# Kernel optimization log

Measured on AMD Instinct MI355X. Metric: run time of the kernel, lower is better.

The kernel has to match this reference:

```python
import jax, jax.numpy as jnp
import numpy as np

P = 16  # patch size

def _conv1x1(w, b, h):
    # w: [O, C], h: [B, C, H, W]
    return jnp.einsum('oc,bcij->boij', w, h) + b[None, :, None, None]

def _forward(x, pe_w, pe_b, mix1_w, mix1_b, mix2_w, mix2_b, qc_w, qc_b,
             codebook, dpre1_w, dpre1_b, dpre2_w, dpre2_b, up_w, up_b):
    B, Cin, H, W = x.shape
    Hp, Wp = H // P, W // P
    # --- encoder: non-overlapping patchify conv (kernel=stride=P) ---
    xp = x.reshape(B, Cin, Hp, P, Wp, P)
    h = jnp.einsum('bcipjq,ocpq->boij', xp, pe_w) + pe_b[None, :, None, None]
    h = jax.nn.relu(h)
    h = jax.nn.relu(_conv1x1(mix1_w, mix1_b, h))
    h = _conv1x1(mix2_w, mix2_b, h)
    # quantize_conv_b
    e = _conv1x1(qc_w, qc_b, h)                      # [B, D, Hp, Wp]
    D = e.shape[1]
    z = e.transpose(0, 2, 3, 1).reshape(B, Hp * Wp, D)   # [B, N, D]
    # --- vector quantization: euclidean argmin over codebook ---
    # dist[b,n,k] = |z|^2 - 2 z.c_k + |c_k|^2
    dist = ((z * z).sum(-1, keepdims=True)
            - 2.0 * jnp.einsum('bnd,kd->bnk', z, codebook)
            + (codebook * codebook).sum(-1))
    idx = jnp.argmin(dist, axis=-1)                  # [B, N] int
    q = codebook[idx]                                # [B, N, D]
    # commitment loss (quantize detached, as in VectorQuantize)
    diff = jnp.mean(jnp.square(jax.lax.stop_gradient(q) - z))
    # straight-through estimator
    q = z + jax.lax.stop_gradient(q - z)
    quant = q.reshape(B, Hp, Wp, D).transpose(0, 3, 1, 2)  # [B, D, Hp, Wp]
    # --- decoder ---
    h = jax.nn.relu(_conv1x1(dpre1_w, dpre1_b, quant))
    h = jax.nn.relu(_conv1x1(dpre2_w, dpre2_b, h))
    # unpatchify: ConvTranspose2d kernel=stride=P, torch weight [C, out, P, P]
    Cout = up_w.shape[1]
    dec = jnp.einsum('bcij,copq->boipjq', h, up_w).reshape(B, Cout, Hp * P, Wp * P)
    dec = dec + up_b[None, :, None, None]
    return dec, diff[None], idx

def setup_inputs() -> dict:
    key = jax.random.key(0)
    ks = jax.random.split(key, 16)
    B, Cin, H, W = 32, 3, 256, 256
    C, D, K = 256, 512, 8192
    s = 0.02
    f32 = jnp.float32
    return {
        'x':       jax.random.normal(ks[0], (B, Cin, H, W), f32),
        'pe_w':    jax.random.normal(ks[1], (C, Cin, P, P), f32) * s,
        'pe_b':    jnp.zeros((C,), f32),
        'mix1_w':  jax.random.normal(ks[2], (C, C), f32) * s,
        'mix1_b':  jnp.zeros((C,), f32),
        'mix2_w':  jax.random.normal(ks[3], (C, C), f32) * s,
        'mix2_b':  jnp.zeros((C,), f32),
        'qc_w':    jax.random.normal(ks[4], (D, C), f32) * s,
        'qc_b':    jnp.zeros((D,), f32),
        'codebook': jax.random.normal(ks[5], (K, D), f32),
        'dpre1_w': jax.random.normal(ks[6], (C, D), f32) * s,
        'dpre1_b': jnp.zeros((C,), f32),
        'dpre2_w': jax.random.normal(ks[7], (C, C), f32) * s,
        'dpre2_b': jnp.zeros((C,), f32),
        'up_w':    jax.random.normal(ks[8], (C, Cin, P, P), f32) * s,
        'up_b':    jnp.zeros((Cin,), f32),
    }

def reference(x, pe_w, pe_b, mix1_w, mix1_b, mix2_w, mix2_b, qc_w, qc_b,
              codebook, dpre1_w, dpre1_b, dpre2_w, dpre2_b, up_w, up_b):
    return _forward(x, pe_w, pe_b, mix1_w, mix1_b, mix2_w, mix2_b, qc_w, qc_b,
                    codebook, dpre1_w, dpre1_b, dpre2_w, dpre2_b, up_w, up_b)
```

## Files before the change

kernel.cpp:

```cpp
#include <hip/hip_runtime.h>
#include <hip/hip_bf16.h>
#include <float.h>


#define TOK   8192
#define CBK   8192
#define CBD   512

typedef short  short8v __attribute__((ext_vector_type(8)));
typedef float  f32x4   __attribute__((ext_vector_type(4)));
typedef unsigned short ush;

__device__ __forceinline__ unsigned short f2bf(float x) {
    union { __hip_bfloat16 b; unsigned short u; } c;
    c.b = __float2bfloat16(x);
    return c.u;
}
__device__ __forceinline__ float bf2f(unsigned short h) {
    return __uint_as_float((unsigned)h << 16);
}

__device__ __forceinline__ void gload16(const void* g, void* l) {
    __builtin_amdgcn_global_load_lds(
        (const __attribute__((address_space(1))) unsigned int*)g,
        (__attribute__((address_space(3))) unsigned int*)l, 16, 0, 0);
}

template<int NPASS, int AMODE, int STMODE, bool RELU>
__global__ __launch_bounds__(256)
void gemm_bf2(const ush* __restrict__ Ah, const ush* __restrict__ Al,
              const ush* __restrict__ Bh, const ush* __restrict__ Bl,
              const float* __restrict__ bias,
              float* __restrict__ Cf, ush* __restrict__ Ch, ush* __restrict__ Cl,
              const float* __restrict__ rowidx, int N, int K, int NT)
{
    __shared__ __align__(16) ush AzH[2][128 * 64];
    __shared__ __align__(16) ush AzL[2][128 * 64];
    __shared__ __align__(16) ush BcH[2][64 * 64];
    __shared__ __align__(16) ush BcL[2][64 * 64];

    const int tid = threadIdx.x, lane = tid & 63, wid = tid >> 6;
    const int wr = wid >> 1, wc = wid & 1;
    const int m0 = blockIdx.x * 128, n0 = blockIdx.y * 64;
    const int l15 = lane & 15, l4 = lane >> 4;

    size_t aoff[4];
    int    aldst[4];
    #pragma unroll
    for (int i = 0; i < 4; ++i) {
        const int ci = (wid * 4 + i) * 64 + lane;
        const int r = ci >> 3, p = ci & 7;
        size_t rowbase;
        if constexpr (AMODE == 2) rowbase = (size_t)((int)rowidx[m0 + r]) * K;
        else                      rowbase = (size_t)(m0 + r) * K;
        aoff[i]  = rowbase + ((p ^ (r & 7)) << 3);
        aldst[i] = (wid * 4 + i) * 512;
    }
    size_t boff[2];
    int    bldst[2];
    #pragma unroll
    for (int i = 0; i < 2; ++i) {
        const int ci = (wid * 2 + i) * 64 + lane;
        const int r = ci >> 3, p = ci & 7;
        boff[i]  = (size_t)(n0 + r) * K + ((p ^ (r & 7)) << 3);
        bldst[i] = (wid * 2 + i) * 512;
    }

    auto STAGE = [&](int t, int b) {
        const int k0 = t << 6;
        #pragma unroll
        for (int i = 0; i < 4; ++i) {
            gload16(Ah + aoff[i] + k0, &AzH[b][aldst[i]]);
            gload16(Al + aoff[i] + k0, &AzL[b][aldst[i]]);
        }
        #pragma unroll
        for (int i = 0; i < 2; ++i) {
            gload16(Bh + boff[i] + k0, &BcH[b][bldst[i]]);
            gload16(Bl + boff[i] + k0, &BcL[b][bldst[i]]);
        }
    };

    f32x4 acc[4][2];
    #pragma unroll
    for (int mi = 0; mi < 4; ++mi)
        #pragma unroll
        for (int nj = 0; nj < 2; ++nj)
            acc[mi][nj] = (f32x4){0.f, 0.f, 0.f, 0.f};

    STAGE(0, 0);
    __syncthreads();
    for (int t = 0; t < NT; ++t) {
        const int b = t & 1;
        if (t + 1 < NT) STAGE(t + 1, b ^ 1);
        #pragma unroll
        for (int ks = 0; ks < 2; ++ks) {
            short8v aFh[4], aFl[4];
            #pragma unroll
            for (int mi = 0; mi < 4; ++mi) {
                const int r = wr * 64 + mi * 16 + l15;
                const int off = r * 64 + (((ks * 4 + l4) ^ (r & 7)) << 3);
                aFh[mi] = *(const short8v*)(&AzH[b][off]);
                aFl[mi] = *(const short8v*)(&AzL[b][off]);
            }
            #pragma unroll
            for (int nj = 0; nj < 2; ++nj) {
                const int rn = wc * 32 + nj * 16 + l15;
                const int off = rn * 64 + (((ks * 4 + l4) ^ (rn & 7)) << 3);
                const short8v bh = *(const short8v*)(&BcH[b][off]);
                const short8v bl = *(const short8v*)(&BcL[b][off]);
                #pragma unroll
                for (int mi = 0; mi < 4; ++mi) {
                    acc[mi][nj] = __builtin_amdgcn_mfma_f32_16x16x32_bf16(aFh[mi], bh, acc[mi][nj], 0, 0, 0);
                    acc[mi][nj] = __builtin_amdgcn_mfma_f32_16x16x32_bf16(aFh[mi], bl, acc[mi][nj], 0, 0, 0);
                    acc[mi][nj] = __builtin_amdgcn_mfma_f32_16x16x32_bf16(aFl[mi], bh, acc[mi][nj], 0, 0, 0);
                    if constexpr (NPASS == 4)
                        acc[mi][nj] = __builtin_amdgcn_mfma_f32_16x16x32_bf16(aFl[mi], bl, acc[mi][nj], 0, 0, 0);
                }
            }
        }
        __syncthreads();
    }

    #pragma unroll
    for (int nj = 0; nj < 2; ++nj) {
        const int n = n0 + wc * 32 + nj * 16 + l15;
        const float bv = (STMODE == 2) ? bias[n >> 8] : bias[n];
        #pragma unroll
        for (int mi = 0; mi < 4; ++mi) {
            #pragma unroll
            for (int i = 0; i < 4; ++i) {
                const int m = m0 + wr * 64 + mi * 16 + l4 * 4 + i;
                float v = acc[mi][nj][i] + bv;
                if constexpr (RELU) v = fmaxf(v, 0.f);
                if constexpr (STMODE == 0) {
                    const unsigned short h = f2bf(v);
                    Ch[(size_t)m * N + n] = h;
                    Cl[(size_t)m * N + n] = f2bf(v - bf2f(h));
                } else if constexpr (STMODE == 1) {
                    Cf[(size_t)m * N + n] = v;
                    Ch[(size_t)m * N + n] = f2bf(v);
                } else {
                    const int o = n >> 8, p = (n >> 4) & 15, q = n & 15;
                    const int b2 = m >> 8, ii = (m >> 4) & 15, jj = m & 15;
                    Cf[((size_t)(b2 * 3 + o) * 256 + ii * 16 + p) * 256 + jj * 16 + q] = v;
                }
            }
        }
    }
}

__global__ __launch_bounds__(256)
void vq_scan(const ush* __restrict__ zh, const ush* __restrict__ cbh,
             const float* __restrict__ cnorm, int* __restrict__ cand)
{
    __shared__ __align__(16) ush Az[2][128 * 64];
    __shared__ __align__(16) ush Bc[2][128 * 64];

    const int tid = threadIdx.x, lane = tid & 63, wid = tid >> 6;
    const int wr = wid >> 1, wc = wid & 1;
    const int m0 = blockIdx.x * 128;
    const int cy = blockIdx.y;
    const int l15 = lane & 15, l4 = lane >> 4;

    size_t soff[4];
    int    ldst[4];
    #pragma unroll
    for (int i = 0; i < 4; ++i) {
        const int ci = (wid * 4 + i) * 64 + lane;
        const int r = ci >> 3, p = ci & 7;
        soff[i] = (size_t)r * CBD + ((p ^ (r & 7)) << 3);
        ldst[i] = (wid * 4 + i) * 512;
    }

    auto STAGE = [&](int t, int b) {
        const int chk = t >> 3, k0 = (t & 7) << 6;
        const size_t ab = (size_t)m0 * CBD + k0;
        const size_t bb = (size_t)(cy * 1024 + chk * 128) * CBD + k0;
        #pragma unroll
        for (int i = 0; i < 4; ++i) {
            gload16(zh  + ab + soff[i], &Az[b][ldst[i]]);
            gload16(cbh + bb + soff[i], &Bc[b][ldst[i]]);
        }
    };

    float r1[16], r2[16];
    int   i1[16], i2[16];
    #pragma unroll
    for (int r = 0; r < 16; ++r) { r1[r] = FLT_MAX; r2[r] = FLT_MAX; i1[r] = 0; i2[r] = 0; }

    f32x4 acc[4][4];
    STAGE(0, 0);
    __syncthreads();
    for (int t = 0; t < 64; ++t) {
        const int b = t & 1;
        if (t < 63) STAGE(t + 1, b ^ 1);
        if ((t & 7) == 0) {
            #pragma unroll
            for (int mi = 0; mi < 4; ++mi)
                #pragma unroll
                for (int nj = 0; nj < 4; ++nj)
                    acc[mi][nj] = (f32x4){0.f, 0.f, 0.f, 0.f};
        }
        #pragma unroll
        for (int ks = 0; ks < 2; ++ks) {
            short8v aF[4];
            #pragma unroll
            for (int mi = 0; mi < 4; ++mi) {
                const int r = wr * 64 + mi * 16 + l15;
                aF[mi] = *(const short8v*)(&Az[b][r * 64 + (((ks * 4 + l4) ^ (r & 7)) << 3)]);
            }
            #pragma unroll
            for (int nj = 0; nj < 4; ++nj) {
                const int rn = wc * 64 + nj * 16 + l15;
                const short8v bF = *(const short8v*)(&Bc[b][rn * 64 + (((ks * 4 + l4) ^ (rn & 7)) << 3)]);
                #pragma unroll
                for (int mi = 0; mi < 4; ++mi)
                    acc[mi][nj] = __builtin_amdgcn_mfma_f32_16x16x32_bf16(aF[mi], bF, acc[mi][nj], 0, 0, 0);
            }
        }
        if ((t & 7) == 7) {
            const int c0 = cy * 1024 + (t >> 3) * 128;
            #pragma unroll
            for (int nj = 0; nj < 4; ++nj) {
                const int code = c0 + wc * 64 + nj * 16 + l15;
                const float cn = cnorm[code];
                #pragma unroll
                for (int mi = 0; mi < 4; ++mi) {
                    #pragma unroll
                    for (int i = 0; i < 4; ++i) {
                        const float d = cn - 2.0f * acc[mi][nj][i];
                        const int rr = mi * 4 + i;
                        if (d < r1[rr]) { r2[rr] = r1[rr]; i2[rr] = i1[rr]; r1[rr] = d; i1[rr] = code; }
                        else if (d < r2[rr]) { r2[rr] = d; i2[rr] = code; }
                    }
                }
            }
        }
        __syncthreads();
    }

    #pragma unroll
    for (int r = 0; r < 16; ++r) {
        float a1 = r1[r], a2 = r2[r];
        int   x1 = i1[r], x2 = i2[r];
        #pragma unroll
        for (int off = 1; off < 16; off <<= 1) {
            const float b1 = __shfl_xor(a1, off), b2 = __shfl_xor(a2, off);
            const int   y1 = __shfl_xor(x1, off), y2 = __shfl_xor(x2, off);
            if (b1 < a1) {
                const float n2 = (a1 < b2) ? a1 : b2;
                const int   m2 = (a1 < b2) ? x1 : y2;
                a2 = n2; x2 = m2; a1 = b1; x1 = y1;
            } else {
                if (b1 < a2) { a2 = b1; x2 = y1; }
            }
        }
        r1[r] = a1; i1[r] = x1; r2[r] = a2; i2[r] = x2;
    }
    if (l15 == 0) {
        const int slot = cy * 2 + wc;
        #pragma unroll
        for (int mi = 0; mi < 4; ++mi)
            #pragma unroll
            for (int i = 0; i < 4; ++i) {
                const int tok = m0 + wr * 64 + mi * 16 + l4 * 4 + i;
                cand[(slot * 2 + 0) * TOK + tok] = i1[mi * 4 + i];
                cand[(slot * 2 + 1) * TOK + tok] = i2[mi * 4 + i];
            }
    }
}

__global__ __launch_bounds__(256)
void exact_select(const float* __restrict__ z, const float* __restrict__ cb,
                  const int* __restrict__ cand, int ncand,
                  float* __restrict__ idx_out, float* __restrict__ diffp)
{
    const int t    = blockIdx.x * 4 + (threadIdx.x >> 6);
    const int lane = threadIdx.x & 63;

    const float4 za = *(const float4*)(z + (size_t)t * CBD + lane * 8);
    const float4 zb = *(const float4*)(z + (size_t)t * CBD + lane * 8 + 4);
    const double zd[8] = {za.x, za.y, za.z, za.w, zb.x, zb.y, zb.z, zb.w};

    double bestd = DBL_MAX;
    int    besti = 0x7fffffff;
    for (int c = 0; c < ncand; ++c) {
        const int code = cand[c * TOK + t];
        const float4 ca  = *(const float4*)(cb + (size_t)code * CBD + lane * 8);
        const float4 cbv = *(const float4*)(cb + (size_t)code * CBD + lane * 8 + 4);
        const double cd[8] = {ca.x, ca.y, ca.z, ca.w, cbv.x, cbv.y, cbv.z, cbv.w};
        double s = 0.0;
        #pragma unroll
        for (int j = 0; j < 8; ++j) { const double d = cd[j] - zd[j]; s = fma(d, d, s); }
        #pragma unroll
        for (int off = 32; off >= 1; off >>= 1) s += __shfl_down(s, off);
        s = __shfl(s, 0);
        if (s < bestd || (s == bestd && code < besti)) { bestd = s; besti = code; }
    }
    if (lane == 0) {
        idx_out[t] = (float)besti;
        atomicAdd(diffp, (float)(bestd * (1.0 / ((double)TOK * CBD))));
    }
}

__global__ __launch_bounds__(256)
void cb_norm(const float* __restrict__ cb, float* __restrict__ cnorm)
{
    const int row  = blockIdx.x * 4 + (threadIdx.x >> 6);
    const int lane = threadIdx.x & 63;
    const float4* p = (const float4*)(cb + (size_t)row * CBD + lane * 8);
    const float4 a = p[0], b = p[1];
    double s = (double)a.x*a.x + (double)a.y*a.y + (double)a.z*a.z + (double)a.w*a.w
             + (double)b.x*b.x + (double)b.y*b.y + (double)b.z*b.z + (double)b.w*b.w;
    #pragma unroll
    for (int off = 32; off >= 1; off >>= 1) s += __shfl_down(s, off);
    if (lane == 0) cnorm[row] = (float)s;
}

__global__ __launch_bounds__(256)
void split_hl(const float* __restrict__ src, ush* __restrict__ h, ush* __restrict__ l)
{
    const size_t i8 = (size_t)blockIdx.x * 256 + threadIdx.x;
    const float4 a = *(const float4*)(src + i8 * 8);
    const float4 b = *(const float4*)(src + i8 * 8 + 4);
    const float xs[8] = {a.x, a.y, a.z, a.w, b.x, b.y, b.z, b.w};
    union { unsigned short u[8]; short8v v; } H, L;
    #pragma unroll
    for (int j = 0; j < 8; ++j) {
        const unsigned short hh = f2bf(xs[j]);
        H.u[j] = hh;
        L.u[j] = f2bf(xs[j] - bf2f(hh));
    }
    *(short8v*)(h + i8 * 8) = H.v;
    *(short8v*)(l + i8 * 8) = L.v;
}

__global__ __launch_bounds__(256)
void split_x(const float* __restrict__ x, ush* __restrict__ xh, ush* __restrict__ xl)
{
    const int i8 = blockIdx.x * 256 + threadIdx.x;
    const int m = i8 / 96, kc = (i8 % 96) * 8;
    const int b = m >> 8, ii = (m >> 4) & 15, jj = m & 15;
    const int c = kc >> 8, p = (kc >> 4) & 15, q = kc & 15;
    const float* src = x + ((size_t)(b * 3 + c) * 256 + ii * 16 + p) * 256 + jj * 16 + q;
    const float4 a = *(const float4*)src;
    const float4 d = *(const float4*)(src + 4);
    const float xs[8] = {a.x, a.y, a.z, a.w, d.x, d.y, d.z, d.w};
    union { unsigned short u[8]; short8v v; } H, L;
    #pragma unroll
    for (int j = 0; j < 8; ++j) {
        const unsigned short hh = f2bf(xs[j]);
        H.u[j] = hh;
        L.u[j] = f2bf(xs[j] - bf2f(hh));
    }
    *(short8v*)(xh + (size_t)i8 * 8) = H.v;
    *(short8v*)(xl + (size_t)i8 * 8) = L.v;
}

__global__ __launch_bounds__(256)
void transpose_upw_split(const float* __restrict__ up_w, ush* __restrict__ th, ush* __restrict__ tl)
{
    const int id = blockIdx.x * 256 + threadIdx.x;
    const int n = id >> 8, c = id & 255;
    const float v = up_w[c * 768 + n];
    const unsigned short h = f2bf(v);
    th[id] = h;
    tl[id] = f2bf(v - bf2f(h));
}

extern "C" void kernel_launch(void* const* d_in, const int* in_sizes, int n_in,
                              void* d_out, int out_size, void* d_ws, size_t ws_size,
                              hipStream_t stream)
{
    const float* x        = (const float*)d_in[0];
    const float* pe_w     = (const float*)d_in[1];
    const float* pe_b     = (const float*)d_in[2];
    const float* mix1_w   = (const float*)d_in[3];
    const float* mix1_b   = (const float*)d_in[4];
    const float* mix2_w   = (const float*)d_in[5];
    const float* mix2_b   = (const float*)d_in[6];
    const float* qc_w     = (const float*)d_in[7];
    const float* qc_b     = (const float*)d_in[8];
    const float* codebook = (const float*)d_in[9];
    const float* dpre1_w  = (const float*)d_in[10];
    const float* dpre1_b  = (const float*)d_in[11];
    const float* dpre2_w  = (const float*)d_in[12];
    const float* dpre2_b  = (const float*)d_in[13];
    const float* up_w     = (const float*)d_in[14];
    const float* up_b     = (const float*)d_in[15];

    char* W = (char*)d_ws;
    ush*   hAh  = (ush*)(W + 0);
    ush*   hAl  = (ush*)(W + 4194304);
    ush*   hBh  = (ush*)(W + 8388608);
    ush*   hBl  = (ush*)(W + 12582912);
    ush*   xph  = (ush*)(W + 16777216);
    ush*   xpl  = (ush*)(W + 29360128);
    float* z    = (float*)(W + 16777216);
    ush*   zh   = (ush*)(W + 33554432);
    ush*   cbh  = (ush*)(W + 41943040);
    ush*   cbl  = (ush*)(W + 50331648);
    ush*   peh  = (ush*)(W + 58720256);
    ush*   pel  = (ush*)(W + 59113472);
    ush*   m1h  = (ush*)(W + 59506688);
    ush*   m1l  = (ush*)(W + 59637760);
    ush*   m2h  = (ush*)(W + 59768832);
    ush*   m2l  = (ush*)(W + 59899904);
    ush*   qch  = (ush*)(W + 60030976);
    ush*   qcl  = (ush*)(W + 60293120);
    ush*   d1h  = (ush*)(W + 60555264);
    ush*   d1l  = (ush*)(W + 60817408);
    ush*   d2h  = (ush*)(W + 61079552);
    ush*   d2l  = (ush*)(W + 61210624);
    ush*   uTh  = (ush*)(W + 61341696);
    ush*   uTl  = (ush*)(W + 61734912);
    float* cnorm= (float*)(W + 62128128);
    int*   cand = (int*)(W + 62160896);

    float* dec     = (float*)d_out;
    float* diffp   = dec + 6291456;
    float* idx_out = (float*)d_out + 6291457;

    split_hl<<<96,   256, 0, stream>>>(pe_w,    peh, pel);
    split_hl<<<32,   256, 0, stream>>>(mix1_w,  m1h, m1l);
    split_hl<<<32,   256, 0, stream>>>(mix2_w,  m2h, m2l);
    split_hl<<<64,   256, 0, stream>>>(qc_w,    qch, qcl);
    split_hl<<<64,   256, 0, stream>>>(dpre1_w, d1h, d1l);
    split_hl<<<32,   256, 0, stream>>>(dpre2_w, d2h, d2l);
    split_hl<<<2048, 256, 0, stream>>>(codebook, cbh, cbl);
    split_x<<<3072,  256, 0, stream>>>(x, xph, xpl);
    transpose_upw_split<<<768, 256, 0, stream>>>(up_w, uTh, uTl);
    cb_norm<<<2048, 256, 0, stream>>>(codebook, cnorm);

    gemm_bf2<4, 0, 0, true ><<<dim3(64, 4),  256, 0, stream>>>(xph, xpl, peh, pel, pe_b,   nullptr, hAh, hAl, nullptr, 256, 768, 12);
    gemm_bf2<4, 0, 0, true ><<<dim3(64, 4),  256, 0, stream>>>(hAh, hAl, m1h, m1l, mix1_b, nullptr, hBh, hBl, nullptr, 256, 256, 4);
    gemm_bf2<4, 0, 0, false><<<dim3(64, 4),  256, 0, stream>>>(hBh, hBl, m2h, m2l, mix2_b, nullptr, hAh, hAl, nullptr, 256, 256, 4);
    gemm_bf2<4, 0, 1, false><<<dim3(64, 8),  256, 0, stream>>>(hAh, hAl, qch, qcl, qc_b,   z,       zh,  nullptr, nullptr, 512, 256, 4);

    vq_scan<<<dim3(64, 8), 256, 0, stream>>>(zh, cbh, cnorm, cand);
    hipMemsetAsync(diffp, 0, sizeof(float), stream);
    exact_select<<<TOK / 4, 256, 0, stream>>>(z, codebook, cand, 32, idx_out, diffp);

    gemm_bf2<3, 2, 0, true ><<<dim3(64, 4),  256, 0, stream>>>(cbh, cbl, d1h, d1l, dpre1_b, nullptr, hAh, hAl, idx_out, 256, 512, 8);
    gemm_bf2<3, 0, 0, true ><<<dim3(64, 4),  256, 0, stream>>>(hAh, hAl, d2h, d2l, dpre2_b, nullptr, hBh, hBl, nullptr, 256, 256, 4);
    gemm_bf2<3, 0, 2, false><<<dim3(64, 12), 256, 0, stream>>>(hBh, hBl, uTh, uTl, up_b,    dec,     nullptr, nullptr, nullptr, 768, 256, 4);
}
```

Before: 722.1 us.

## Remap GEMM and VQ scan workgroups to 1D grids with XCD-aware swizzle

GEMM and vq_scan launches move from 2D to 1D grids. Block ids are remapped so that consecutive blocks dispatched round-robin to the 8 XCDs are grouped per XCD, aiming to keep tiles that share A or B data in the same L2. The six small weight-split launches are merged into one kernel to cut launch overhead. The remap assumes a grid size divisible by 64 and 8, which holds for every launch here.

```diff
diff --git a/kernel.cpp b/kernel.cpp
--- a/kernel.cpp
+++ b/kernel.cpp
@@ -41,7 +41,11 @@
 
     const int tid = threadIdx.x, lane = tid & 63, wid = tid >> 6;
     const int wr = wid >> 1, wc = wid & 1;
-    const int m0 = blockIdx.x * 128, n0 = blockIdx.y * 64;
+    const int nwg = gridDim.x;
+    const int ny  = nwg >> 6;
+    const int q   = nwg >> 3;
+    const int lid = (blockIdx.x & 7) * q + (blockIdx.x >> 3);
+    const int m0  = (lid / ny) * 128, n0 = (lid % ny) * 64;
     const int l15 = lane & 15, l4 = lane >> 4;
 
     size_t aoff[4];
@@ -140,9 +144,9 @@
                     Cf[(size_t)m * N + n] = v;
                     Ch[(size_t)m * N + n] = f2bf(v);
                 } else {
-                    const int o = n >> 8, p = (n >> 4) & 15, q = n & 15;
+                    const int o = n >> 8, p = (n >> 4) & 15, qq = n & 15;
                     const int b2 = m >> 8, ii = (m >> 4) & 15, jj = m & 15;
-                    Cf[((size_t)(b2 * 3 + o) * 256 + ii * 16 + p) * 256 + jj * 16 + q] = v;
+                    Cf[((size_t)(b2 * 3 + o) * 256 + ii * 16 + p) * 256 + jj * 16 + qq] = v;
                 }
             }
         }
@@ -158,8 +162,8 @@
 
     const int tid = threadIdx.x, lane = tid & 63, wid = tid >> 6;
     const int wr = wid >> 1, wc = wid & 1;
-    const int m0 = blockIdx.x * 128;
-    const int cy = blockIdx.y;
+    const int cy = blockIdx.x & 7;
+    const int m0 = (blockIdx.x >> 3) * 128;
     const int l15 = lane & 15, l4 = lane >> 4;
 
     size_t soff[4];
@@ -317,10 +321,9 @@
     if (lane == 0) cnorm[row] = (float)s;
 }
 
-__global__ __launch_bounds__(256)
-void split_hl(const float* __restrict__ src, ush* __restrict__ h, ush* __restrict__ l)
-{
-    const size_t i8 = (size_t)blockIdx.x * 256 + threadIdx.x;
+__device__ __forceinline__ void split8(const float* __restrict__ src, size_t i8,
+                                       ush* __restrict__ h, ush* __restrict__ l)
+{
     const float4 a = *(const float4*)(src + i8 * 8);
     const float4 b = *(const float4*)(src + i8 * 8 + 4);
     const float xs[8] = {a.x, a.y, a.z, a.w, b.x, b.y, b.z, b.w};
@@ -333,6 +336,30 @@
     }
     *(short8v*)(h + i8 * 8) = H.v;
     *(short8v*)(l + i8 * 8) = L.v;
+}
+
+__global__ __launch_bounds__(256)
+void split_hl(const float* __restrict__ src, ush* __restrict__ h, ush* __restrict__ l)
+{
+    split8(src, (size_t)blockIdx.x * 256 + threadIdx.x, h, l);
+}
+
+__global__ __launch_bounds__(256)
+void split_weights(const float* __restrict__ pe_w,  const float* __restrict__ m1w,
+                   const float* __restrict__ m2w,   const float* __restrict__ qcw,
+                   const float* __restrict__ d1w,   const float* __restrict__ d2w,
+                   ush* peh, ush* pel, ush* m1h, ush* m1l, ush* m2h, ush* m2l,
+                   ush* qch, ush* qcl, ush* d1h, ush* d1l, ush* d2h, ush* d2l)
+{
+    const int b = blockIdx.x;
+    const float* src; ush *h, *l; int base;
+    if      (b < 96)  { src = pe_w; h = peh; l = pel; base = b; }
+    else if (b < 128) { src = m1w;  h = m1h; l = m1l; base = b - 96; }
+    else if (b < 160) { src = m2w;  h = m2h; l = m2l; base = b - 128; }
+    else if (b < 224) { src = qcw;  h = qch; l = qcl; base = b - 160; }
+    else if (b < 288) { src = d1w;  h = d1h; l = d1l; base = b - 224; }
+    else              { src = d2w;  h = d2h; l = d2l; base = b - 288; }
+    split8(src, (size_t)base * 256 + threadIdx.x, h, l);
 }
 
 __global__ __launch_bounds__(256)
@@ -421,27 +448,24 @@
     float* diffp   = dec + 6291456;
     float* idx_out = (float*)d_out + 6291457;
 
-    split_hl<<<96,   256, 0, stream>>>(pe_w,    peh, pel);
-    split_hl<<<32,   256, 0, stream>>>(mix1_w,  m1h, m1l);
-    split_hl<<<32,   256, 0, stream>>>(mix2_w,  m2h, m2l);
-    split_hl<<<64,   256, 0, stream>>>(qc_w,    qch, qcl);
-    split_hl<<<64,   256, 0, stream>>>(dpre1_w, d1h, d1l);
-    split_hl<<<32,   256, 0, stream>>>(dpre2_w, d2h, d2l);
+    split_weights<<<320, 256, 0, stream>>>(pe_w, mix1_w, mix2_w, qc_w, dpre1_w, dpre2_w,
+                                           peh, pel, m1h, m1l, m2h, m2l,
+                                           qch, qcl, d1h, d1l, d2h, d2l);
     split_hl<<<2048, 256, 0, stream>>>(codebook, cbh, cbl);
     split_x<<<3072,  256, 0, stream>>>(x, xph, xpl);
     transpose_upw_split<<<768, 256, 0, stream>>>(up_w, uTh, uTl);
     cb_norm<<<2048, 256, 0, stream>>>(codebook, cnorm);
 
-    gemm_bf2<4, 0, 0, true ><<<dim3(64, 4),  256, 0, stream>>>(xph, xpl, peh, pel, pe_b,   nullptr, hAh, hAl, nullptr, 256, 768, 12);
-    gemm_bf2<4, 0, 0, true ><<<dim3(64, 4),  256, 0, stream>>>(hAh, hAl, m1h, m1l, mix1_b, nullptr, hBh, hBl, nullptr, 256, 256, 4);
-    gemm_bf2<4, 0, 0, false><<<dim3(64, 4),  256, 0, stream>>>(hBh, hBl, m2h, m2l, mix2_b, nullptr, hAh, hAl, nullptr, 256, 256, 4);
-    gemm_bf2<4, 0, 1, false><<<dim3(64, 8),  256, 0, stream>>>(hAh, hAl, qch, qcl, qc_b,   z,       zh,  nullptr, nullptr, 512, 256, 4);
-
-    vq_scan<<<dim3(64, 8), 256, 0, stream>>>(zh, cbh, cnorm, cand);
+    gemm_bf2<4, 0, 0, true ><<<256, 256, 0, stream>>>(xph, xpl, peh, pel, pe_b,   nullptr, hAh, hAl, nullptr, 256, 768, 12);
+    gemm_bf2<4, 0, 0, true ><<<256, 256, 0, stream>>>(hAh, hAl, m1h, m1l, mix1_b, nullptr, hBh, hBl, nullptr, 256, 256, 4);
+    gemm_bf2<4, 0, 0, false><<<256, 256, 0, stream>>>(hBh, hBl, m2h, m2l, mix2_b, nullptr, hAh, hAl, nullptr, 256, 256, 4);
+    gemm_bf2<4, 0, 1, false><<<512, 256, 0, stream>>>(hAh, hAl, qch, qcl, qc_b,   z,       zh,  nullptr, nullptr, 512, 256, 4);
+
+    vq_scan<<<512, 256, 0, stream>>>(zh, cbh, cnorm, cand);
     hipMemsetAsync(diffp, 0, sizeof(float), stream);
     exact_select<<<TOK / 4, 256, 0, stream>>>(z, codebook, cand, 32, idx_out, diffp);
 
-    gemm_bf2<3, 2, 0, true ><<<dim3(64, 4),  256, 0, stream>>>(cbh, cbl, d1h, d1l, dpre1_b, nullptr, hAh, hAl, idx_out, 256, 512, 8);
-    gemm_bf2<3, 0, 0, true ><<<dim3(64, 4),  256, 0, stream>>>(hAh, hAl, d2h, d2l, dpre2_b, nullptr, hBh, hBl, nullptr, 256, 256, 4);
-    gemm_bf2<3, 0, 2, false><<<dim3(64, 12), 256, 0, stream>>>(hBh, hBl, uTh, uTl, up_b,    dec,     nullptr, nullptr, nullptr, 768, 256, 4);
-}
+    gemm_bf2<3, 2, 0, true ><<<256, 256, 0, stream>>>(cbh, cbl, d1h, d1l, dpre1_b, nullptr, hAh, hAl, idx_out, 256, 512, 8);
+    gemm_bf2<3, 0, 0, true ><<<256, 256, 0, stream>>>(hAh, hAl, d2h, d2l, dpre2_b, nullptr, hBh, hBl, nullptr, 256, 256, 4);
+    gemm_bf2<3, 0, 2, false><<<768, 256, 0, stream>>>(hBh, hBl, uTh, uTl, up_b,    dec,     nullptr, nullptr, nullptr, 768, 256, 4);
+}
```

After: 719.9 us. About the same (-0.3%).
